# Optimization experiments

Measured on AMD Instinct MI355X. Metric: run time of the kernel, lower is better.

Reference implementation:

```python
import jax, jax.numpy as jnp
import numpy as np

C = 256
HEADS = 8
HD = C // HEADS
WS = 7
SCALE = HD ** -0.5
EPS = 1e-5


def _ln(x, g, b):
    m = jnp.mean(x, axis=-1, keepdims=True)
    v = jnp.var(x, axis=-1, keepdims=True)
    return (x - m) * jax.lax.rsqrt(v + EPS) * g + b


def setup_inputs() -> dict:
    key = jax.random.key(0)
    ks = jax.random.split(key, 8)
    B, H, W = 32, 56, 56
    N = H * W
    hid = 4 * C
    s = lambda fan: 1.0 / np.sqrt(fan)
    return {
        "x": jax.random.normal(ks[0], (B, N, C), dtype=jnp.float32),
        "ln1_g": jnp.ones((C,), jnp.float32),
        "ln1_b": jnp.zeros((C,), jnp.float32),
        "qkv_w": jax.random.normal(ks[1], (C, 3 * C), jnp.float32) * s(C),
        "qkv_b": jnp.zeros((3 * C,), jnp.float32),
        "ln2_g": jnp.ones((C,), jnp.float32),
        "ln2_b": jnp.zeros((C,), jnp.float32),
        "fc1_w": jax.random.normal(ks[2], (C, hid), jnp.float32) * s(C),
        "fc1_b": jnp.zeros((hid,), jnp.float32),
        "mlp_ln_g": jnp.ones((hid,), jnp.float32),
        "mlp_ln_b": jnp.zeros((hid,), jnp.float32),
        "fc2_w": jax.random.normal(ks[3], (hid, C), jnp.float32) * s(hid),
        "fc2_b": jnp.zeros((C,), jnp.float32),
        "H": H,
        "W": W,
    }


def _lsa(x, qkv_w, qkv_b, H, W):
    # x: (B, N, C); H, W divisible by WS -> padding is zero (matches torch path)
    B, N, _ = x.shape
    hp, wp = H // WS, W // WS
    P = hp * wp
    # window partition: (B, P, WS*WS, C)
    xw = x.reshape(B, hp, WS, wp, WS, C).transpose(0, 1, 3, 2, 4, 5).reshape(B, P, WS * WS, C)
    qkv = xw @ qkv_w + qkv_b                      # (B, P, 49, 3C)
    qkv = qkv.reshape(B, P, WS * WS, 3, HEADS, HD).transpose(3, 0, 1, 4, 2, 5)
    q, k, v = qkv[0], qkv[1], qkv[2]              # (B, P, heads, 49, HD)
    attn = jax.nn.softmax(jnp.einsum('bphqd,bphkd->bphqk', q * SCALE, k), axis=-1)
    out = jnp.einsum('bphqk,bphkd->bphqd', attn, v)
    # merge heads, un-window: note LSA never applies self.proj (faithful)
    out = out.transpose(0, 1, 3, 2, 4).reshape(B, hp, wp, WS, WS, C)
    out = out.transpose(0, 1, 3, 2, 4, 5).reshape(B, N, C)
    return out


def reference(x, ln1_g, ln1_b, qkv_w, qkv_b, ln2_g, ln2_b,
              fc1_w, fc1_b, mlp_ln_g, mlp_ln_b, fc2_w, fc2_b, H, W):
    x = x + _lsa(_ln(x, ln1_g, ln1_b), qkv_w, qkv_b, H, W)
    h = _ln(x, ln2_g, ln2_b)
    h = jax.nn.gelu(h @ fc1_w + fc1_b, approximate=False)
    h = _ln(h, mlp_ln_g, mlp_ln_b)
    x = x + (h @ fc2_w + fc2_b)
    return x
```

## Files before the change

kernel.cpp:

```cpp
#include <hip/hip_runtime.h>
#include <cmath>

typedef __bf16 bf16;
typedef __bf16 bf16x4 __attribute__((ext_vector_type(4)));
typedef __bf16 bf16x8 __attribute__((ext_vector_type(8)));
typedef float floatx4 __attribute__((ext_vector_type(4)));

constexpr int BATCH = 32;
constexpr int NTOK  = 3136;
constexpr int CDIM  = 256;
constexpr int MROWS = BATCH * NTOK;
constexpr int HIDD  = 1024;
constexpr float ATTN_SCALE = 0.17677669529663689f;

__device__ __forceinline__ float gelu_fast(float x) {
    float p = fmaf(0.044715f * x, x * x, x);
    return __fdividef(x, 1.0f + __expf(-1.5957691216057308f * p));
}

__device__ __forceinline__ void load8(const bf16* p, float* o) {
    bf16x8 v = *reinterpret_cast<const bf16x8*>(p);
#pragma unroll
    for (int j = 0; j < 8; j++) o[j] = (float)v[j];
}

__device__ __forceinline__ void gload_lds16(const void* g, void* l) {
    __builtin_amdgcn_global_load_lds(
        (const __attribute__((address_space(1))) void*)g,
        (__attribute__((address_space(3))) void*)l, 16, 0, 0);
}

__global__ __launch_bounds__(256) void wt_kernel(
    const float* __restrict__ Win, bf16* __restrict__ Wt, int Ksz, int Nsz)
{
    int id = blockIdx.x * 256 + threadIdx.x;
    int n = id / Ksz, k = id % Ksz;
    Wt[id] = (bf16)Win[(size_t)k * Nsz + n];
}

__global__ __launch_bounds__(256) void ln_apply_f32_kernel(
    const float* __restrict__ X, const float* __restrict__ g,
    const float* __restrict__ b, bf16* __restrict__ Y)
{
    int tok  = (blockIdx.x * 256 + threadIdx.x) >> 6;
    int lane = threadIdx.x & 63;
    const float* row = X + (size_t)tok * CDIM;
    float4 v = *reinterpret_cast<const float4*>(row + lane * 4);
    float s  = v.x + v.y + v.z + v.w;
    float ss = v.x * v.x + v.y * v.y + v.z * v.z + v.w * v.w;
#pragma unroll
    for (int off = 32; off > 0; off >>= 1) {
        s  += __shfl_xor(s,  off, 64);
        ss += __shfl_xor(ss, off, 64);
    }
    float mean = s * (1.0f / CDIM);
    float var  = ss * (1.0f / CDIM) - mean * mean;
    if (var < 0.f) var = 0.f;
    float rstd = rsqrtf(var + 1e-5f);
    float4 gg = *reinterpret_cast<const float4*>(g + lane * 4);
    float4 bb = *reinterpret_cast<const float4*>(b + lane * 4);
    bf16x4 o;
    o[0] = (bf16)((v.x - mean) * rstd * gg.x + bb.x);
    o[1] = (bf16)((v.y - mean) * rstd * gg.y + bb.y);
    o[2] = (bf16)((v.z - mean) * rstd * gg.z + bb.z);
    o[3] = (bf16)((v.w - mean) * rstd * gg.w + bb.w);
    *reinterpret_cast<bf16x4*>(Y + (size_t)tok * CDIM + lane * 4) = o;
}

__global__ __launch_bounds__(256) void ln_inplace_h_kernel(
    bf16* __restrict__ H, const float* __restrict__ g, const float* __restrict__ b)
{
    int tok  = (blockIdx.x * 256 + threadIdx.x) >> 6;
    int lane = threadIdx.x & 63;
    bf16* row = H + (size_t)tok * HIDD;
    float f[16];
    load8(row + lane * 8, f);
    load8(row + 512 + lane * 8, f + 8);
    float s = 0.f, ss = 0.f;
#pragma unroll
    for (int j = 0; j < 16; j++) { s += f[j]; ss += f[j] * f[j]; }
#pragma unroll
    for (int off = 32; off > 0; off >>= 1) {
        s  += __shfl_xor(s,  off, 64);
        ss += __shfl_xor(ss, off, 64);
    }
    float mean = s * (1.0f / HIDD);
    float var  = ss * (1.0f / HIDD) - mean * mean;
    if (var < 0.f) var = 0.f;
    float rstd = rsqrtf(var + 1e-5f);
    bf16x8 o0, o1;
#pragma unroll
    for (int j = 0; j < 8; j++) {
        o0[j] = (bf16)((f[j]     - mean) * rstd * g[lane * 8 + j]       + b[lane * 8 + j]);
        o1[j] = (bf16)((f[j + 8] - mean) * rstd * g[512 + lane * 8 + j] + b[512 + lane * 8 + j]);
    }
    *reinterpret_cast<bf16x8*>(row + lane * 8) = o0;
    *reinterpret_cast<bf16x8*>(row + 512 + lane * 8) = o1;
}

template<int EPI, typename TO>
__global__ __launch_bounds__(256) void gemm_bt_kernel(
    const bf16* __restrict__ A, const bf16* __restrict__ Bt,
    const float* __restrict__ bias, const float* __restrict__ resid,
    TO* __restrict__ out, int Nsz, int Ksz)
{
    __shared__ bf16 lA[128 * 64];
    __shared__ bf16 lB[128 * 64];
    const int t = threadIdx.x;
    const int lane = t & 63, w = t >> 6;
    const int quad = lane >> 4, l16 = lane & 15;
    const int wm = (w >> 1) * 64, wn = (w & 1) * 64;

    const int gx   = gridDim.x;
    const int flat = blockIdx.y * gx + blockIdx.x;
    const int cpx  = (gx * gridDim.y) >> 3;
    const int fl2  = (flat & 7) * cpx + (flat >> 3);
    const int bx   = fl2 % gx, by = fl2 / gx;

    const size_t m0 = (size_t)by * 128;
    const int n0 = bx * 128;
    const int srow = w * 32 + (lane >> 3);
    const int scol = (lane & 7) * 8;

    floatx4 acc[4][4] = {};

    for (int kc = 0; kc < Ksz; kc += 64) {
#pragma unroll
        for (int j = 0; j < 4; j++) {
            gload_lds16(A  + (m0 + srow + j * 8) * Ksz + kc + scol, &lA[(w * 32 + j * 8) * 64]);
            gload_lds16(Bt + (size_t)(n0 + srow + j * 8) * Ksz + kc + scol, &lB[(w * 32 + j * 8) * 64]);
        }
        __syncthreads();
#pragma unroll
        for (int ks = 0; ks < 64; ks += 32) {
            bf16x8 af[4], bfv[4];
#pragma unroll
            for (int i = 0; i < 4; i++) {
                af[i]  = *reinterpret_cast<const bf16x8*>(&lA[(wm + i * 16 + l16) * 64 + ks + quad * 8]);
                bfv[i] = *reinterpret_cast<const bf16x8*>(&lB[(wn + i * 16 + l16) * 64 + ks + quad * 8]);
            }
#pragma unroll
            for (int mi = 0; mi < 4; mi++)
#pragma unroll
                for (int ni = 0; ni < 4; ni++)
                    acc[mi][ni] = __builtin_amdgcn_mfma_f32_16x16x32_bf16(af[mi], bfv[ni], acc[mi][ni], 0, 0, 0);
        }
        __syncthreads();
    }

#pragma unroll
    for (int mi = 0; mi < 4; mi++) {
#pragma unroll
        for (int ni = 0; ni < 4; ni++) {
            int col = n0 + wn + ni * 16 + l16;
            float bcol = bias[col];
#pragma unroll
            for (int r = 0; r < 4; r++) {
                size_t row = m0 + wm + mi * 16 + quad * 4 + r;
                float v = acc[mi][ni][r] + bcol;
                if (EPI == 1) v = gelu_fast(v);
                if (EPI == 2) v += resid[row * (size_t)Nsz + col];
                out[row * (size_t)Nsz + col] = (TO)v;
            }
        }
    }
}

__global__ __launch_bounds__(256) void attn_kernel(
    const bf16* __restrict__ qkv, const float* __restrict__ X,
    float* __restrict__ x1)
{
    __shared__ bf16 pbuf[4][64 * 72];
    __shared__ bf16 vtbuf[4][32 * 72];
    const int w = threadIdx.x >> 6, lane = threadIdx.x & 63;
    const int quad = lane >> 4, l16 = lane & 15;
    const int blk = blockIdx.x;
    const int hg = blk & 1, p = (blk >> 1) & 63, b = blk >> 7;
    const int h = hg * 4 + w;
    const int py = p >> 3, px = p & 7;
    const size_t gbase = (size_t)b * NTOK + py * 7 * 56 + px * 7;
    bf16* P  = pbuf[w];
    bf16* VT = vtbuf[w];

    unsigned int* vz = (unsigned int*)VT;
    for (int i = lane; i < 32 * 72 / 2; i += 64) vz[i] = 0u;

    for (int idx = lane; idx < 49 * 4; idx += 64) {
        int tk = idx >> 2, d8 = (idx & 3) * 8;
        size_t g = gbase + (tk / 7) * 56 + (tk % 7);
        bf16x8 vv = *reinterpret_cast<const bf16x8*>(qkv + g * 768 + 512 + h * 32 + d8);
#pragma unroll
        for (int j = 0; j < 8; j++) VT[(d8 + j) * 72 + tk] = vv[j];
    }

    bf16x8 qf[4], kf[4];
#pragma unroll
    for (int mt = 0; mt < 4; mt++) {
        int i = mt * 16 + l16; if (i > 48) i = 48;
        size_t g = gbase + (i / 7) * 56 + (i % 7);
        qf[mt] = *reinterpret_cast<const bf16x8*>(qkv + g * 768 +       h * 32 + quad * 8);
        kf[mt] = *reinterpret_cast<const bf16x8*>(qkv + g * 768 + 256 + h * 32 + quad * 8);
    }

    floatx4 s[4][4];
#pragma unroll
    for (int mt = 0; mt < 4; mt++)
#pragma unroll
        for (int nt = 0; nt < 4; nt++) {
            floatx4 z = {};
            s[mt][nt] = __builtin_amdgcn_mfma_f32_16x16x32_bf16(qf[mt], kf[nt], z, 0, 0, 0);
        }

#pragma unroll
    for (int mt = 0; mt < 4; mt++) {
#pragma unroll
        for (int r = 0; r < 4; r++) {
            float mx = -1e30f;
#pragma unroll
            for (int nt = 0; nt < 4; nt++) {
                int col = nt * 16 + l16;
                float v = (col < 49) ? s[mt][nt][r] * ATTN_SCALE : -1e30f;
                s[mt][nt][r] = v;
                mx = fmaxf(mx, v);
            }
#pragma unroll
            for (int off = 1; off < 16; off <<= 1) mx = fmaxf(mx, __shfl_xor(mx, off, 64));
            float sum = 0.f;
#pragma unroll
            for (int nt = 0; nt < 4; nt++) {
                float e = __expf(s[mt][nt][r] - mx);
                s[mt][nt][r] = e;
                sum += e;
            }
#pragma unroll
            for (int off = 1; off < 16; off <<= 1) sum += __shfl_xor(sum, off, 64);
            float inv = 1.0f / sum;
            int prow = mt * 16 + quad * 4 + r;
#pragma unroll
            for (int nt = 0; nt < 4; nt++)
                P[prow * 72 + nt * 16 + l16] = (bf16)(s[mt][nt][r] * inv);
        }
    }

    __syncthreads();

    floatx4 o[4][2] = {};
#pragma unroll
    for (int ks = 0; ks < 2; ks++) {
        bf16x8 pf[4], vf[2];
#pragma unroll
        for (int mt = 0; mt < 4; mt++)
            pf[mt] = *reinterpret_cast<const bf16x8*>(&P[(mt * 16 + l16) * 72 + ks * 32 + quad * 8]);
#pragma unroll
        for (int nt = 0; nt < 2; nt++)
            vf[nt] = *reinterpret_cast<const bf16x8*>(&VT[(nt * 16 + l16) * 72 + ks * 32 + quad * 8]);
#pragma unroll
        for (int mt = 0; mt < 4; mt++)
#pragma unroll
            for (int nt = 0; nt < 2; nt++)
                o[mt][nt] = __builtin_amdgcn_mfma_f32_16x16x32_bf16(pf[mt], vf[nt], o[mt][nt], 0, 0, 0);
    }

#pragma unroll
    for (int mt = 0; mt < 4; mt++) {
#pragma unroll
        for (int r = 0; r < 4; r++) {
            int i = mt * 16 + quad * 4 + r;
            if (i < 49) {
                size_t g = gbase + (i / 7) * 56 + (i % 7);
#pragma unroll
                for (int nt = 0; nt < 2; nt++) {
                    size_t adr = g * CDIM + h * 32 + nt * 16 + l16;
                    x1[adr] = X[adr] + o[mt][nt][r];
                }
            }
        }
    }
}

extern "C" void kernel_launch(void* const* d_in, const int* in_sizes, int n_in,
                              void* d_out, int out_size, void* d_ws, size_t ws_size,
                              hipStream_t stream) {
    const float* x      = (const float*)d_in[0];
    const float* ln1_g  = (const float*)d_in[1];
    const float* ln1_b  = (const float*)d_in[2];
    const float* qkv_w  = (const float*)d_in[3];
    const float* qkv_b  = (const float*)d_in[4];
    const float* ln2_g  = (const float*)d_in[5];
    const float* ln2_b  = (const float*)d_in[6];
    const float* fc1_w  = (const float*)d_in[7];
    const float* fc1_b  = (const float*)d_in[8];
    const float* mlp_g  = (const float*)d_in[9];
    const float* mlp_b  = (const float*)d_in[10];
    const float* fc2_w  = (const float*)d_in[11];
    const float* fc2_b  = (const float*)d_in[12];
    float* out = (float*)d_out;

    char* ws = (char*)d_ws;
    bf16* qkv_wt = (bf16*)ws;  ws += (size_t)768 * 256 * 2;
    bf16* fc1_wt = (bf16*)ws;  ws += (size_t)1024 * 256 * 2;
    bf16* fc2_wt = (bf16*)ws;  ws += (size_t)256 * 1024 * 2;
    bf16* xn     = (bf16*)ws;  ws += (size_t)MROWS * CDIM * 2;
    bf16* qkvb   = (bf16*)ws;
    bf16* hbuf   = (bf16*)ws;
    float* x1 = out;

    wt_kernel<<<768,  256, 0, stream>>>(qkv_w, qkv_wt, 256, 768);
    wt_kernel<<<1024, 256, 0, stream>>>(fc1_w, fc1_wt, 256, 1024);
    wt_kernel<<<1024, 256, 0, stream>>>(fc2_w, fc2_wt, 1024, 256);

    ln_apply_f32_kernel<<<MROWS / 4, 256, 0, stream>>>(x, ln1_g, ln1_b, xn);
    gemm_bt_kernel<0, bf16><<<dim3(768 / 128, MROWS / 128), 256, 0, stream>>>(
        xn, qkv_wt, qkv_b, nullptr, qkvb, 768, 256);
    attn_kernel<<<BATCH * 64 * 2, 256, 0, stream>>>(qkvb, x, x1);
    ln_apply_f32_kernel<<<MROWS / 4, 256, 0, stream>>>(x1, ln2_g, ln2_b, xn);
    gemm_bt_kernel<1, bf16><<<dim3(HIDD / 128, MROWS / 128), 256, 0, stream>>>(
        xn, fc1_wt, fc1_b, nullptr, hbuf, HIDD, 256);
    ln_inplace_h_kernel<<<MROWS / 4, 256, 0, stream>>>(hbuf, mlp_g, mlp_b);
    gemm_bt_kernel<2, float><<<dim3(CDIM / 128, MROWS / 128), 256, 0, stream>>>(
        hbuf, fc2_wt, fc2_b, x1, out, CDIM, 1024);
}
```

Measured before the change: 756.7 us.

## Fold MLP LayerNorm into fc2 GEMM epilogue via precomputed stats and weights

Replaces the in-place LayerNorm over the hidden activations with a stats-only pass that stores per-row mean and rstd. Gamma is folded into the transposed fc2 weights, and column constants (beta·W, gamma·W) are precomputed so the fc2 epilogue applies the normalization algebraically. This removes one full write of the large hidden buffer. It risks extra numerical error from cancellation, and the path is taken only when the workspace is big enough.

```diff
diff --git a/kernel.cpp b/kernel.cpp
--- a/kernel.cpp
+++ b/kernel.cpp
@@ -31,11 +31,39 @@
 }
 
 __global__ __launch_bounds__(256) void wt_kernel(
-    const float* __restrict__ Win, bf16* __restrict__ Wt, int Ksz, int Nsz)
+    const float* __restrict__ Win, bf16* __restrict__ Wt, int Ksz, int Nsz,
+    const float* __restrict__ gsc)
 {
     int id = blockIdx.x * 256 + threadIdx.x;
     int n = id / Ksz, k = id % Ksz;
-    Wt[id] = (bf16)Win[(size_t)k * Nsz + n];
+    float v = Win[(size_t)k * Nsz + n];
+    if (gsc) v *= gsc[k];
+    Wt[id] = (bf16)v;
+}
+
+__global__ __launch_bounds__(256) void c12_part_kernel(
+    const float* __restrict__ W, const float* __restrict__ g,
+    const float* __restrict__ b, float2* __restrict__ part)
+{
+    int n = threadIdx.x, j = blockIdx.x;
+    float c1 = 0.f, c2 = 0.f;
+#pragma unroll 8
+    for (int k = j * 64; k < j * 64 + 64; k++) {
+        float w = W[(size_t)k * 256 + n];
+        c1 = fmaf(b[k], w, c1);
+        c2 = fmaf(g[k], w, c2);
+    }
+    part[j * 256 + n] = make_float2(c1, c2);
+}
+
+__global__ __launch_bounds__(256) void c12_red_kernel(
+    const float2* __restrict__ part, float2* __restrict__ c12)
+{
+    int n = threadIdx.x;
+    float c1 = 0.f, c2 = 0.f;
+#pragma unroll
+    for (int j = 0; j < 16; j++) { float2 p = part[j * 256 + n]; c1 += p.x; c2 += p.y; }
+    c12[n] = make_float2(c1, c2);
 }
 
 __global__ __launch_bounds__(256) void ln_apply_f32_kernel(
@@ -67,6 +95,29 @@
     *reinterpret_cast<bf16x4*>(Y + (size_t)tok * CDIM + lane * 4) = o;
 }
 
+__global__ __launch_bounds__(256) void hstats_kernel(
+    const bf16* __restrict__ H, float2* __restrict__ mr)
+{
+    int tok  = (blockIdx.x * 256 + threadIdx.x) >> 6;
+    int lane = threadIdx.x & 63;
+    const bf16* row = H + (size_t)tok * HIDD;
+    float f[16];
+    load8(row + lane * 8, f);
+    load8(row + 512 + lane * 8, f + 8);
+    float s = 0.f, ss = 0.f;
+#pragma unroll
+    for (int j = 0; j < 16; j++) { s += f[j]; ss += f[j] * f[j]; }
+#pragma unroll
+    for (int off = 32; off > 0; off >>= 1) {
+        s  += __shfl_xor(s,  off, 64);
+        ss += __shfl_xor(ss, off, 64);
+    }
+    float mean = s * (1.0f / HIDD);
+    float var  = ss * (1.0f / HIDD) - mean * mean;
+    if (var < 0.f) var = 0.f;
+    if (lane == 0) mr[tok] = make_float2(mean, rsqrtf(var + 1e-5f));
+}
+
 __global__ __launch_bounds__(256) void ln_inplace_h_kernel(
     bf16* __restrict__ H, const float* __restrict__ g, const float* __restrict__ b)
 {
@@ -102,7 +153,8 @@
 __global__ __launch_bounds__(256) void gemm_bt_kernel(
     const bf16* __restrict__ A, const bf16* __restrict__ Bt,
     const float* __restrict__ bias, const float* __restrict__ resid,
-    TO* __restrict__ out, int Nsz, int Ksz)
+    TO* __restrict__ out, int Nsz, int Ksz,
+    const float2* __restrict__ mr, const float2* __restrict__ c12)
 {
     __shared__ bf16 lA[128 * 64];
     __shared__ bf16 lB[128 * 64];
@@ -148,18 +200,41 @@
         __syncthreads();
     }
 
+    float bcol[4];
+    float2 cc[4];
+#pragma unroll
+    for (int ni = 0; ni < 4; ni++) {
+        int col = n0 + wn + ni * 16 + l16;
+        bcol[ni] = bias[col];
+        if (EPI == 2) cc[ni] = c12[col];
+    }
+
 #pragma unroll
     for (int mi = 0; mi < 4; mi++) {
 #pragma unroll
-        for (int ni = 0; ni < 4; ni++) {
-            int col = n0 + wn + ni * 16 + l16;
-            float bcol = bias[col];
-#pragma unroll
-            for (int r = 0; r < 4; r++) {
-                size_t row = m0 + wm + mi * 16 + quad * 4 + r;
-                float v = acc[mi][ni][r] + bcol;
-                if (EPI == 1) v = gelu_fast(v);
-                if (EPI == 2) v += resid[row * (size_t)Nsz + col];
+        for (int r = 0; r < 4; r++) {
+            size_t row = m0 + wm + mi * 16 + quad * 4 + r;
+            float sc = 0.f, ofs = 0.f;
+            if (EPI == 2) {
+                float2 mv = mr[row];
+                sc  = mv.y;
+                ofs = -mv.x * mv.y;
+            }
+#pragma unroll
+            for (int ni = 0; ni < 4; ni++) {
+                int col = n0 + wn + ni * 16 + l16;
+                float v;
+                if (EPI == 0) {
+                    v = acc[mi][ni][r] + bcol[ni];
+                } else if (EPI == 1) {
+                    v = gelu_fast(acc[mi][ni][r] + bcol[ni]);
+                } else if (EPI == 2) {
+                    float base = fmaf(ofs, cc[ni].y, cc[ni].x + bcol[ni]);
+                    v = fmaf(sc, acc[mi][ni][r], base);
+                    v += resid[row * (size_t)Nsz + col];
+                } else {
+                    v = acc[mi][ni][r] + bcol[ni] + resid[row * (size_t)Nsz + col];
+                }
                 out[row * (size_t)Nsz + col] = (TO)v;
             }
         }
@@ -302,21 +377,43 @@
     bf16* fc2_wt = (bf16*)ws;  ws += (size_t)256 * 1024 * 2;
     bf16* xn     = (bf16*)ws;  ws += (size_t)MROWS * CDIM * 2;
     bf16* qkvb   = (bf16*)ws;
-    bf16* hbuf   = (bf16*)ws;
+    bf16* hbuf   = (bf16*)ws;  ws += (size_t)MROWS * HIDD * 2;
+
+    const size_t base_bytes = (size_t)(ws - (char*)d_ws);
+    const size_t tail_bytes = (size_t)MROWS * sizeof(float2)
+                            + (size_t)16 * 256 * sizeof(float2)
+                            + (size_t)256 * sizeof(float2);
+    const bool fuse_ln = (ws_size >= base_bytes + tail_bytes);
+
+    float2* mr   = (float2*)ws;
+    float2* c12p = mr + MROWS;
+    float2* c12  = c12p + 16 * 256;
     float* x1 = out;
 
-    wt_kernel<<<768,  256, 0, stream>>>(qkv_w, qkv_wt, 256, 768);
-    wt_kernel<<<1024, 256, 0, stream>>>(fc1_w, fc1_wt, 256, 1024);
-    wt_kernel<<<1024, 256, 0, stream>>>(fc2_w, fc2_wt, 1024, 256);
+    wt_kernel<<<768,  256, 0, stream>>>(qkv_w, qkv_wt, 256, 768, nullptr);
+    wt_kernel<<<1024, 256, 0, stream>>>(fc1_w, fc1_wt, 256, 1024, nullptr);
+    wt_kernel<<<1024, 256, 0, stream>>>(fc2_w, fc2_wt, 1024, 256,
+                                        fuse_ln ? mlp_g : nullptr);
+    if (fuse_ln) {
+        c12_part_kernel<<<16, 256, 0, stream>>>(fc2_w, mlp_g, mlp_b, c12p);
+        c12_red_kernel<<<1, 256, 0, stream>>>(c12p, c12);
+    }
 
     ln_apply_f32_kernel<<<MROWS / 4, 256, 0, stream>>>(x, ln1_g, ln1_b, xn);
     gemm_bt_kernel<0, bf16><<<dim3(768 / 128, MROWS / 128), 256, 0, stream>>>(
-        xn, qkv_wt, qkv_b, nullptr, qkvb, 768, 256);
+        xn, qkv_wt, qkv_b, nullptr, qkvb, 768, 256, nullptr, nullptr);
     attn_kernel<<<BATCH * 64 * 2, 256, 0, stream>>>(qkvb, x, x1);
     ln_apply_f32_kernel<<<MROWS / 4, 256, 0, stream>>>(x1, ln2_g, ln2_b, xn);
     gemm_bt_kernel<1, bf16><<<dim3(HIDD / 128, MROWS / 128), 256, 0, stream>>>(
-        xn, fc1_wt, fc1_b, nullptr, hbuf, HIDD, 256);
-    ln_inplace_h_kernel<<<MROWS / 4, 256, 0, stream>>>(hbuf, mlp_g, mlp_b);
-    gemm_bt_kernel<2, float><<<dim3(CDIM / 128, MROWS / 128), 256, 0, stream>>>(
-        hbuf, fc2_wt, fc2_b, x1, out, CDIM, 1024);
-}
+        xn, fc1_wt, fc1_b, nullptr, hbuf, HIDD, 256, nullptr, nullptr);
+
+    if (fuse_ln) {
+        hstats_kernel<<<MROWS / 4, 256, 0, stream>>>(hbuf, mr);
+        gemm_bt_kernel<2, float><<<dim3(CDIM / 128, MROWS / 128), 256, 0, stream>>>(
+            hbuf, fc2_wt, fc2_b, x1, out, CDIM, 1024, mr, c12);
+    } else {
+        ln_inplace_h_kernel<<<MROWS / 4, 256, 0, stream>>>(hbuf, mlp_g, mlp_b);
+        gemm_bt_kernel<3, float><<<dim3(CDIM / 128, MROWS / 128), 256, 0, stream>>>(
+            hbuf, fc2_wt, fc2_b, x1, out, CDIM, 1024, nullptr, nullptr);
+    }
+}
```

After: 719.8 us. 1.05x faster.

## Fuse MLP fc1-GELU-LayerNorm-fc2 into one kernel with algebraic LN folding

Applied to the files above, without the earlier changes.

Replaces the fc1 GEMM, in-place hidden LayerNorm and fc2 GEMM with a single kernel that keeps each 128-token hidden tile in LDS and accumulates fc2 directly. The LayerNorm over the hidden dimension is folded algebraically: gamma is pre-multiplied into the fc2 weights, and per-column constants sum(b*W) and sum(g*W) are precomputed so mean and rstd are applied in the epilogue from row statistics gathered during GELU. It also adds an XOR swizzle to LDS tiles, baked into the weight transpose and LN output layouts, to reduce bank conflicts. This removes the round trip of the large bf16 hidden buffer through HBM, at the cost of high register pressure, less parallelism (one block per 128 rows), and a fallback path that depends on workspace size.

```diff
diff --git a/kernel.cpp b/kernel.cpp
--- a/kernel.cpp
+++ b/kernel.cpp
@@ -31,16 +31,45 @@
 }
 
 __global__ __launch_bounds__(256) void wt_kernel(
-    const float* __restrict__ Win, bf16* __restrict__ Wt, int Ksz, int Nsz)
+    const float* __restrict__ Win, bf16* __restrict__ Wt, int Ksz, int Nsz,
+    const float* __restrict__ gsc, int swz)
 {
     int id = blockIdx.x * 256 + threadIdx.x;
     int n = id / Ksz, k = id % Ksz;
-    Wt[id] = (bf16)Win[(size_t)k * Nsz + n];
+    float v = Win[(size_t)k * Nsz + n];
+    if (gsc) v *= gsc[k];
+    int kp = k ^ (swz & ((n & 7) << 3));
+    Wt[(size_t)n * Ksz + kp] = (bf16)v;
+}
+
+__global__ __launch_bounds__(256) void c12_part_kernel(
+    const float* __restrict__ W, const float* __restrict__ g,
+    const float* __restrict__ b, float2* __restrict__ part)
+{
+    int n = threadIdx.x, j = blockIdx.x;
+    float c1 = 0.f, c2 = 0.f;
+#pragma unroll 8
+    for (int k = j * 64; k < j * 64 + 64; k++) {
+        float w = W[(size_t)k * 256 + n];
+        c1 = fmaf(b[k], w, c1);
+        c2 = fmaf(g[k], w, c2);
+    }
+    part[j * 256 + n] = make_float2(c1, c2);
+}
+
+__global__ __launch_bounds__(256) void c12_red_kernel(
+    const float2* __restrict__ part, float2* __restrict__ c12)
+{
+    int n = threadIdx.x;
+    float c1 = 0.f, c2 = 0.f;
+#pragma unroll
+    for (int j = 0; j < 16; j++) { float2 p = part[j * 256 + n]; c1 += p.x; c2 += p.y; }
+    c12[n] = make_float2(c1, c2);
 }
 
 __global__ __launch_bounds__(256) void ln_apply_f32_kernel(
     const float* __restrict__ X, const float* __restrict__ g,
-    const float* __restrict__ b, bf16* __restrict__ Y)
+    const float* __restrict__ b, bf16* __restrict__ Y, int swz)
 {
     int tok  = (blockIdx.x * 256 + threadIdx.x) >> 6;
     int lane = threadIdx.x & 63;
@@ -64,7 +93,8 @@
     o[1] = (bf16)((v.y - mean) * rstd * gg.y + bb.y);
     o[2] = (bf16)((v.z - mean) * rstd * gg.z + bb.z);
     o[3] = (bf16)((v.w - mean) * rstd * gg.w + bb.w);
-    *reinterpret_cast<bf16x4*>(Y + (size_t)tok * CDIM + lane * 4) = o;
+    int off4 = (lane * 4) ^ (swz & ((tok & 7) << 3));
+    *reinterpret_cast<bf16x4*>(Y + (size_t)tok * CDIM + off4) = o;
 }
 
 __global__ __launch_bounds__(256) void ln_inplace_h_kernel(
@@ -98,7 +128,7 @@
     *reinterpret_cast<bf16x8*>(row + 512 + lane * 8) = o1;
 }
 
-template<int EPI, typename TO>
+template<int EPI, bool SWZ, typename TO>
 __global__ __launch_bounds__(256) void gemm_bt_kernel(
     const bf16* __restrict__ A, const bf16* __restrict__ Bt,
     const float* __restrict__ bias, const float* __restrict__ resid,
@@ -121,6 +151,7 @@
     const int n0 = bx * 128;
     const int srow = w * 32 + (lane >> 3);
     const int scol = (lane & 7) * 8;
+    const int swzr = SWZ ? ((l16 & 7) << 3) : 0;
 
     floatx4 acc[4][4] = {};
 
@@ -136,8 +167,8 @@
             bf16x8 af[4], bfv[4];
 #pragma unroll
             for (int i = 0; i < 4; i++) {
-                af[i]  = *reinterpret_cast<const bf16x8*>(&lA[(wm + i * 16 + l16) * 64 + ks + quad * 8]);
-                bfv[i] = *reinterpret_cast<const bf16x8*>(&lB[(wn + i * 16 + l16) * 64 + ks + quad * 8]);
+                af[i]  = *reinterpret_cast<const bf16x8*>(&lA[(wm + i * 16 + l16) * 64 + ((ks + quad * 8) ^ swzr)]);
+                bfv[i] = *reinterpret_cast<const bf16x8*>(&lB[(wn + i * 16 + l16) * 64 + ((ks + quad * 8) ^ swzr)]);
             }
 #pragma unroll
             for (int mi = 0; mi < 4; mi++)
@@ -159,8 +190,161 @@
                 size_t row = m0 + wm + mi * 16 + quad * 4 + r;
                 float v = acc[mi][ni][r] + bcol;
                 if (EPI == 1) v = gelu_fast(v);
-                if (EPI == 2) v += resid[row * (size_t)Nsz + col];
+                if (EPI == 3) v += resid[row * (size_t)Nsz + col];
                 out[row * (size_t)Nsz + col] = (TO)v;
+            }
+        }
+    }
+}
+
+__global__ __launch_bounds__(256, 2) void mlp_fused_kernel(
+    const bf16* __restrict__ A,
+    const bf16* __restrict__ W1t,
+    const bf16* __restrict__ W2t,
+    const float* __restrict__ b1, const float* __restrict__ b2,
+    const float* __restrict__ resid, const float2* __restrict__ c12,
+    float* __restrict__ out)
+{
+    __shared__ bf16 lP[128 * 64 * 2];
+    __shared__ bf16 lH[128 * 128];
+    __shared__ float2 lstats[128][2];
+
+    const int t = threadIdx.x;
+    const int lane = t & 63, w = t >> 6;
+    const int quad = lane >> 4, l16 = lane & 15;
+    const int whid  = (w >> 1) * 64, wtok1 = (w & 1) * 64;
+    const int wtok2 = (w >> 1) * 64, wout  = (w & 1) * 128;
+
+    const int nb  = gridDim.x;
+    const int cpx = nb >> 3;
+    const int bid = (blockIdx.x & 7) * cpx + (blockIdx.x >> 3);
+    const size_t m0 = (size_t)bid * 128;
+
+    const int srow = w * 32 + (lane >> 3);
+    const int scol = (lane & 7) * 8;
+    const int swzr = (l16 & 7) << 3;
+
+    bf16* lX  = lP;
+    bf16* lW1 = lP + 128 * 64;
+    bf16* lW2 = lP;
+
+    floatx4 acc2[4][8] = {};
+    float tsum[4] = {0.f, 0.f, 0.f, 0.f};
+    float tss[4]  = {0.f, 0.f, 0.f, 0.f};
+
+    for (int nc = 0; nc < 8; nc++) {
+        floatx4 sT[4][4] = {};
+        for (int kc = 0; kc < 256; kc += 64) {
+#pragma unroll
+            for (int j = 0; j < 4; j++) {
+                gload_lds16(A   + (m0 + srow + j * 8) * 256 + kc + scol,
+                            &lX[(w * 32 + j * 8) * 64]);
+                gload_lds16(W1t + (size_t)(nc * 128 + srow + j * 8) * 256 + kc + scol,
+                            &lW1[(w * 32 + j * 8) * 64]);
+            }
+            __syncthreads();
+#pragma unroll
+            for (int ks = 0; ks < 64; ks += 32) {
+                bf16x8 wf[4], xf[4];
+#pragma unroll
+                for (int i = 0; i < 4; i++) {
+                    wf[i] = *reinterpret_cast<const bf16x8*>(&lW1[(whid  + i * 16 + l16) * 64 + ((ks + quad * 8) ^ swzr)]);
+                    xf[i] = *reinterpret_cast<const bf16x8*>(&lX [(wtok1 + i * 16 + l16) * 64 + ((ks + quad * 8) ^ swzr)]);
+                }
+#pragma unroll
+                for (int mt = 0; mt < 4; mt++)
+#pragma unroll
+                    for (int nt = 0; nt < 4; nt++)
+                        sT[mt][nt] = __builtin_amdgcn_mfma_f32_16x16x32_bf16(wf[mt], xf[nt], sT[mt][nt], 0, 0, 0);
+            }
+            __syncthreads();
+        }
+#pragma unroll
+        for (int mt = 0; mt < 4; mt++) {
+            float4 b1v = *reinterpret_cast<const float4*>(&b1[nc * 128 + whid + mt * 16 + quad * 4]);
+            const float* b1p = reinterpret_cast<const float*>(&b1v);
+#pragma unroll
+            for (int nt = 0; nt < 4; nt++) {
+                bf16x4 h4;
+#pragma unroll
+                for (int r = 0; r < 4; r++) {
+                    float v = gelu_fast(sT[mt][nt][r] + b1p[r]);
+                    tsum[nt] += v;
+                    tss[nt] = fmaf(v, v, tss[nt]);
+                    h4[r] = (bf16)v;
+                }
+                int tok  = wtok1 + nt * 16 + l16;
+                int hidb = (whid + mt * 16 + quad * 4) ^ swzr;
+                *reinterpret_cast<bf16x4*>(&lH[tok * 128 + hidb]) = h4;
+            }
+        }
+        __syncthreads();
+#pragma unroll
+        for (int k2s = 0; k2s < 2; k2s++) {
+#pragma unroll
+            for (int j = 0; j < 8; j++) {
+                gload_lds16(W2t + (size_t)(w * 64 + j * 8 + (lane >> 3)) * 1024
+                                + nc * 128 + k2s * 64 + scol,
+                            &lW2[(w * 64 + j * 8) * 64]);
+            }
+            __syncthreads();
+#pragma unroll
+            for (int ks2 = 0; ks2 < 64; ks2 += 32) {
+                bf16x8 hf[4], vf[8];
+#pragma unroll
+                for (int i = 0; i < 4; i++)
+                    hf[i] = *reinterpret_cast<const bf16x8*>(
+                        &lH[(wtok2 + i * 16 + l16) * 128 + ((k2s * 64 + ks2 + quad * 8) ^ swzr)]);
+#pragma unroll
+                for (int i = 0; i < 8; i++)
+                    vf[i] = *reinterpret_cast<const bf16x8*>(
+                        &lW2[(wout + i * 16 + l16) * 64 + ((ks2 + quad * 8) ^ swzr)]);
+#pragma unroll
+                for (int mi = 0; mi < 4; mi++)
+#pragma unroll
+                    for (int ni = 0; ni < 8; ni++)
+                        acc2[mi][ni] = __builtin_amdgcn_mfma_f32_16x16x32_bf16(hf[mi], vf[ni], acc2[mi][ni], 0, 0, 0);
+            }
+            __syncthreads();
+        }
+    }
+
+#pragma unroll
+    for (int nt = 0; nt < 4; nt++) {
+        float s = tsum[nt], ss = tss[nt];
+        s  += __shfl_xor(s, 16, 64);  ss += __shfl_xor(ss, 16, 64);
+        s  += __shfl_xor(s, 32, 64);  ss += __shfl_xor(ss, 32, 64);
+        if (quad == 0) lstats[wtok1 + nt * 16 + l16][w >> 1] = make_float2(s, ss);
+    }
+    __syncthreads();
+
+    float bcol[8]; float2 cc[8];
+#pragma unroll
+    for (int ni = 0; ni < 8; ni++) {
+        int col = wout + ni * 16 + l16;
+        bcol[ni] = b2[col];
+        cc[ni] = c12[col];
+    }
+#pragma unroll
+    for (int mi = 0; mi < 4; mi++) {
+#pragma unroll
+        for (int r = 0; r < 4; r++) {
+            int rl = wtok2 + mi * 16 + quad * 4 + r;
+            float2 p0 = lstats[rl][0], p1 = lstats[rl][1];
+            float s = p0.x + p1.x, ss = p0.y + p1.y;
+            float mean = s * (1.0f / HIDD);
+            float var  = ss * (1.0f / HIDD) - mean * mean;
+            if (var < 0.f) var = 0.f;
+            float rstd = rsqrtf(var + 1e-5f);
+            float ofs = -mean * rstd;
+            size_t row = m0 + rl;
+            const float* rr = resid + row * CDIM;
+            float* orow = out + row * CDIM;
+#pragma unroll
+            for (int ni = 0; ni < 8; ni++) {
+                int col = wout + ni * 16 + l16;
+                float v = fmaf(rstd, acc2[mi][ni][r], fmaf(ofs, cc[ni].y, cc[ni].x + bcol[ni]));
+                orow[col] = v + rr[col];
             }
         }
     }
@@ -302,21 +486,44 @@
     bf16* fc2_wt = (bf16*)ws;  ws += (size_t)256 * 1024 * 2;
     bf16* xn     = (bf16*)ws;  ws += (size_t)MROWS * CDIM * 2;
     bf16* qkvb   = (bf16*)ws;
-    bf16* hbuf   = (bf16*)ws;
+    bf16* hbuf   = (bf16*)ws;  ws += (size_t)MROWS * HIDD * 2;
+
+    const size_t base_bytes = (size_t)(ws - (char*)d_ws);
+    const size_t tail_bytes = (size_t)16 * 256 * sizeof(float2) + (size_t)256 * sizeof(float2);
+    const bool fuse = (ws_size >= base_bytes + tail_bytes);
+    const int swz = fuse ? 0x38 : 0;
+
+    float2* c12p = (float2*)ws;
+    float2* c12  = c12p + 16 * 256;
     float* x1 = out;
 
-    wt_kernel<<<768,  256, 0, stream>>>(qkv_w, qkv_wt, 256, 768);
-    wt_kernel<<<1024, 256, 0, stream>>>(fc1_w, fc1_wt, 256, 1024);
-    wt_kernel<<<1024, 256, 0, stream>>>(fc2_w, fc2_wt, 1024, 256);
-
-    ln_apply_f32_kernel<<<MROWS / 4, 256, 0, stream>>>(x, ln1_g, ln1_b, xn);
-    gemm_bt_kernel<0, bf16><<<dim3(768 / 128, MROWS / 128), 256, 0, stream>>>(
-        xn, qkv_wt, qkv_b, nullptr, qkvb, 768, 256);
+    wt_kernel<<<768,  256, 0, stream>>>(qkv_w, qkv_wt, 256, 768, nullptr, swz);
+    wt_kernel<<<1024, 256, 0, stream>>>(fc1_w, fc1_wt, 256, 1024, nullptr, swz);
+    wt_kernel<<<1024, 256, 0, stream>>>(fc2_w, fc2_wt, 1024, 256,
+                                        fuse ? mlp_g : nullptr, swz);
+    if (fuse) {
+        c12_part_kernel<<<16, 256, 0, stream>>>(fc2_w, mlp_g, mlp_b, c12p);
+        c12_red_kernel<<<1, 256, 0, stream>>>(c12p, c12);
+    }
+
+    ln_apply_f32_kernel<<<MROWS / 4, 256, 0, stream>>>(x, ln1_g, ln1_b, xn, swz);
+    if (fuse)
+        gemm_bt_kernel<0, true, bf16><<<dim3(768 / 128, MROWS / 128), 256, 0, stream>>>(
+            xn, qkv_wt, qkv_b, nullptr, qkvb, 768, 256);
+    else
+        gemm_bt_kernel<0, false, bf16><<<dim3(768 / 128, MROWS / 128), 256, 0, stream>>>(
+            xn, qkv_wt, qkv_b, nullptr, qkvb, 768, 256);
     attn_kernel<<<BATCH * 64 * 2, 256, 0, stream>>>(qkvb, x, x1);
-    ln_apply_f32_kernel<<<MROWS / 4, 256, 0, stream>>>(x1, ln2_g, ln2_b, xn);
-    gemm_bt_kernel<1, bf16><<<dim3(HIDD / 128, MROWS / 128), 256, 0, stream>>>(
-        xn, fc1_wt, fc1_b, nullptr, hbuf, HIDD, 256);
-    ln_inplace_h_kernel<<<MROWS / 4, 256, 0, stream>>>(hbuf, mlp_g, mlp_b);
-    gemm_bt_kernel<2, float><<<dim3(CDIM / 128, MROWS / 128), 256, 0, stream>>>(
-        hbuf, fc2_wt, fc2_b, x1, out, CDIM, 1024);
-}
+    ln_apply_f32_kernel<<<MROWS / 4, 256, 0, stream>>>(x1, ln2_g, ln2_b, xn, swz);
+
+    if (fuse) {
+        mlp_fused_kernel<<<MROWS / 128, 256, 0, stream>>>(
+            xn, fc1_wt, fc2_wt, fc1_b, fc2_b, x1, c12, out);
+    } else {
+        gemm_bt_kernel<1, false, bf16><<<dim3(HIDD / 128, MROWS / 128), 256, 0, stream>>>(
+            xn, fc1_wt, fc1_b, nullptr, hbuf, HIDD, 256);
+        ln_inplace_h_kernel<<<MROWS / 4, 256, 0, stream>>>(hbuf, mlp_g, mlp_b);
+        gemm_bt_kernel<3, false, float><<<dim3(CDIM / 128, MROWS / 128), 256, 0, stream>>>(
+            hbuf, fc2_wt, fc2_b, x1, out, CDIM, 1024);
+    }
+}
```

Result: slower. 841.0 us (+11.1%).
